# Kernel optimization log

Hardware: AMD Instinct MI355X
Metric: run time of the kernel (lower is better)

The kernel has to match this reference:

```python
import jax, jax.numpy as jnp
import numpy as np

H, F, K, R = 8, 64, 10, 256  # num_heads, in_features, num_sines, num_realizations
B, L = 4, 2048


def setup_inputs() -> dict:
    key = jax.random.key(0)
    k1, k2, k3, k4, k5, k6 = jax.random.split(key, 6)
    return {
        "queries": jax.random.normal(k1, (B, L, H, F), dtype=jnp.float32),
        "keys": jax.random.normal(k2, (B, L, H, F), dtype=jnp.float32),
        "z": jax.random.normal(k3, (B, H, F, 2 * K, R), dtype=jnp.float32),
        "freqs": jax.random.normal(k4, (H, F, K), dtype=jnp.float32),
        "offsets": jax.random.normal(k5, (H, F, K), dtype=jnp.float32),
        "gains": jax.random.normal(k6, (H, F, K), dtype=jnp.float32),
    }


def reference(queries, keys, z, freqs, offsets, gains):
    h, f_dim, k_sines = freqs.shape
    length = queries.shape[1]
    r = z.shape[-1]
    # split positional / non-positional features (rest is empty here: key_dim == in_features)
    q_pos, q_rest = queries[..., :f_dim], queries[..., f_dim:]
    k_pos, k_rest = keys[..., :f_dim], keys[..., f_dim:]

    idx = jnp.arange(length, dtype=queries.dtype)  # linspace(0, L-1, L)
    fr = jax.nn.sigmoid(freqs)[:, :, None, :] / 2.0          # [H, F, 1, K]
    base = 2.0 * jnp.pi * fr * idx[None, None, :, None]       # [H, F, L, K]
    ph_q = base + offsets[:, :, None, :]
    ph_k = base
    # stack(cos, sin) on last axis then flatten -> interleaved cos0,sin0,... : [H, F, L, 2K]
    omega_q = jnp.stack([jnp.cos(ph_q), jnp.sin(ph_q)], axis=-1).reshape(h, f_dim, length, 2 * k_sines)
    omega_k = jnp.stack([jnp.cos(ph_k), jnp.sin(ph_k)], axis=-1).reshape(h, f_dim, length, 2 * k_sines)

    g = jnp.tile(jax.nn.softplus(gains), (1, 1, 2))           # [H, F, 2K] (block-repeated, as in torch .repeat)
    zs = z * g[None, :, :, :, None] / np.sqrt(r * f_dim).astype(np.float32)  # [B, H, F, 2K, R]

    # fused double contraction over f (in_features) and s (2K sines); equals
    # (omega @ z) permuted then multiplied by queries and summed over in_features
    qhat = jnp.einsum('hfls,bhfsr,blhf->blhr', omega_q, zs, q_pos)  # [B, L, H, R]
    khat = jnp.einsum('hfls,bhfsr,blhf->blhr', omega_k, zs, k_pos)

    qhat = jnp.concatenate([qhat, q_rest], axis=-1)
    khat = jnp.concatenate([khat, k_rest], axis=-1)
    return qhat, khat
```

## Files before the change

### kernel.cpp

```cpp
#include <hip/hip_runtime.h>
#include <math.h>


#define NH 8
#define NF 64
#define NK 10
#define NR 256
#define NB 4
#define NL 2048
#define KTOT 1280
#define BM 128
#define BK 32
#define NCH (KTOT/BK)
#define NFRAG_B 16
#define WS_NEEDED ((size_t)NB*NH*NCH*NFRAG_B*1024)

typedef __attribute__((ext_vector_type(8))) short short8;
typedef __attribute__((ext_vector_type(4))) float f32x4;
typedef __attribute__((ext_vector_type(4))) unsigned int u32x4;
typedef __attribute__((ext_vector_type(2))) unsigned int u32x2;

static __device__ __forceinline__ unsigned short f2b(float f) {
    unsigned x = __float_as_uint(f);
    return (unsigned short)((x + 0x7FFFu + ((x >> 16) & 1u)) >> 16);
}
static __device__ __forceinline__ unsigned int pk2(float a, float b) {
    return (unsigned int)f2b(a) | ((unsigned int)f2b(b) << 16);
}
static __device__ __forceinline__ unsigned int cvtpk(float lo, float hi) {
    unsigned int r;
    asm("v_cvt_pk_bf16_f32 %0, %1, %2" : "=v"(r) : "v"(lo), "v"(hi));
    return r;
}
static __device__ __forceinline__ void gload_lds16(const void* g, void* l) {
    __builtin_amdgcn_global_load_lds(
        (const __attribute__((address_space(1))) unsigned int*)g,
        (__attribute__((address_space(3))) unsigned int*)l, 16, 0, 0);
}

__global__ __launch_bounds__(256)
void spe_prep(const float* __restrict__ z, const float* __restrict__ gains,
              unsigned char* __restrict__ bpack)
{
    __shared__ float s_g[NF*NK];
    const int ch  = blockIdx.x;
    const int bh  = blockIdx.y;
    const int h   = bh & 7;
    const int tid = threadIdx.x;
    for (int i = tid; i < NF*NK; i += 256)
        s_g[i] = log1pf(expf(gains[h*NF*NK + i])) * 0.0078125f;
    __syncthreads();
    const float* zb = z + (size_t)bh * KTOT * NR;
    unsigned char* dst = bpack + ((size_t)(bh*NCH + ch) * NFRAG_B) * 1024;
    #pragma unroll
    for (int it = 0; it < 4; ++it) {
        const int s  = tid + 256*it;
        const int fi = s >> 6;
        const int l  = s & 63;
        const int r  = fi*16 + (l & 15);
        const int k0 = ch*BK + (l >> 4)*8;
        u32x4 wv;
        #pragma unroll
        for (int jp = 0; jp < 4; ++jp) {
            const int ka = k0 + 2*jp, kb = ka + 1;
            const int fa = (ka*3277) >> 16; int sa = ka - fa*20; if (sa >= NK) sa -= NK;
            const int fb = (kb*3277) >> 16; int sb = kb - fb*20; if (sb >= NK) sb -= NK;
            const float va = zb[(size_t)ka*NR + r] * s_g[fa*NK + sa];
            const float vb = zb[(size_t)kb*NR + r] * s_g[fb*NK + sb];
            wv[jp] = pk2(va, vb);
        }
        *(u32x4*)(dst + (size_t)s*16) = wv;
    }
}

#define OFF_B0  0
#define OFF_B1  16384
#define OFF_A   32768
#define OFF_POS 40960
#define OFF_FR  57344
#define OFF_CO  59904
#define OFF_SO  62464
#define SMEM_SZ 65024

__global__ __launch_bounds__(512, 4)
void spe_main(const float* __restrict__ queries, const float* __restrict__ keys,
              const float* __restrict__ freqs, const float* __restrict__ offsets,
              const unsigned char* __restrict__ bpack, float* __restrict__ out)
{
    __shared__ __attribute__((aligned(16))) unsigned char smem[SMEM_SZ];
    const int tid  = threadIdx.x;
    const int lane = tid & 63;
    const int w    = tid >> 6;
    const int l0   = blockIdx.x * 64;
    const int bh   = blockIdx.y;
    const int b = bh >> 3, h = bh & 7;

    float* ld_fr = (float*)(smem + OFF_FR);
    float* ld_co = (float*)(smem + OFF_CO);
    float* ld_so = (float*)(smem + OFF_SO);
    unsigned short* pos_t = (unsigned short*)(smem + OFF_POS);

    for (int i = tid; i < NF*NK; i += 512) {
        const float fv = freqs[h*NF*NK + i];
        ld_fr[i] = 0.5f / (1.0f + expf(-fv));
        const float xo = __builtin_amdgcn_fractf(offsets[h*NF*NK + i] * 0.15915494309189535f);
        ld_co[i] = __builtin_amdgcn_cosf(xo);
        ld_so[i] = __builtin_amdgcn_sinf(xo);
    }
    {
        const int r  = tid >> 2;
        const int f0 = (tid & 3) * 16;
        const int rl = r & 63;
        const float* src = (r < 64)
            ? queries + ((size_t)((b*NL + l0 + rl)*NH + h))*NF + f0
            : keys    + ((size_t)((b*NL + l0 + rl)*NH + h))*NF + f0;
        unsigned short* pdst = pos_t + ((r >> 6) << 12);
        #pragma unroll
        for (int j = 0; j < 4; ++j) {
            const float4 v = *(const float4*)(src + j*4);
            const int f = f0 + j*4;
            pdst[(f+0)*64 + rl] = f2b(v.x);
            pdst[(f+1)*64 + rl] = f2b(v.y);
            pdst[(f+2)*64 + rl] = f2b(v.z);
            pdst[(f+3)*64 + rl] = f2b(v.w);
        }
    }
    __syncthreads();

    const unsigned char* bp = bpack + (size_t)bh * ((size_t)NCH*NFRAG_B*1024);
    const int fi0 = w*2;
    gload_lds16(bp + (size_t)fi0*1024 + lane*16,       smem + OFF_B0 + (fi0  <<10));
    gload_lds16(bp + (size_t)(fi0+1)*1024 + lane*16,   smem + OFF_B0 + ((fi0+1)<<10));

    const int wm = w >> 2, wn = w & 3;
    f32x4 acc[4][4];
    #pragma unroll
    for (int mi = 0; mi < 4; ++mi)
        #pragma unroll
        for (int ni = 0; ni < 4; ++ni)
            acc[mi][ni] = (f32x4){0.f, 0.f, 0.f, 0.f};

    const int rq   = tid & 63;
    const int oct  = (tid >> 6) & 3;
    const int half = tid >> 8;
    const float lf = (float)(l0 + rq);
    const unsigned short* posq = pos_t;
    const unsigned short* posk = pos_t + 4096;
    const int a_log_q = ((rq >> 4) << 10) + ((oct*16 + (rq & 15)) << 4) + (half << 3);
    const int aw_q = a_log_q ^ (((rq >> 4) & 3) << 5);
    const int aw_k = (a_log_q + 4096) ^ (((rq >> 4) & 3) << 5);

    auto synthA = [&](int t, u32x2& q01, u32x2& k01) {
        #pragma unroll
        for (int p = 0; p < 2; ++p) {
            const int kk   = t*BK + oct*8 + (half*2 + p)*2;
            const int f    = (kk*3277) >> 16;
            const int srem = kk - f*20;
            const int kidx = f*NK + (srem >> 1);
            const float x  = __builtin_amdgcn_fractf(ld_fr[kidx] * lf);
            const float ck = __builtin_amdgcn_cosf(x);
            const float sk = __builtin_amdgcn_sinf(x);
            const float co = ld_co[kidx], so = ld_so[kidx];
            const float cq = ck*co - sk*so;
            const float sq = sk*co + ck*so;
            const float pq = __uint_as_float(((unsigned)posq[f*64 + rq]) << 16);
            const float pk = __uint_as_float(((unsigned)posk[f*64 + rq]) << 16);
            q01[p] = cvtpk(cq*pq, sq*pq);
            k01[p] = cvtpk(ck*pk, sk*pk);
        }
    };

    u32x2 q01, k01;
    synthA(0, q01, k01);

    for (int t = 0; t < NCH; ++t) {
        unsigned char* Bcur = smem + ((t & 1) ? OFF_B1 : OFF_B0);
        unsigned char* Bnxt = smem + ((t & 1) ? OFF_B0 : OFF_B1);

        asm volatile("s_waitcnt vmcnt(0)" ::: "memory");
        __builtin_amdgcn_sched_barrier(0);
        __builtin_amdgcn_s_barrier();

        if (t + 1 < NCH) {
            gload_lds16(bp + (size_t)((t+1)*NFRAG_B + fi0)*1024 + lane*16,
                        Bnxt + (fi0<<10));
            gload_lds16(bp + (size_t)((t+1)*NFRAG_B + fi0+1)*1024 + lane*16,
                        Bnxt + ((fi0+1)<<10));
        }

        *(u32x2*)(smem + OFF_A + aw_q) = q01;
        *(u32x2*)(smem + OFF_A + aw_k) = k01;
        asm volatile("s_waitcnt lgkmcnt(0)" ::: "memory");
        __builtin_amdgcn_sched_barrier(0);
        __builtin_amdgcn_s_barrier();

        short8 bf[4];
        #pragma unroll
        for (int ni = 0; ni < 4; ++ni)
            bf[ni] = *(const short8*)(Bcur + ((wn*4 + ni) << 10) + (lane << 4));

        if (t + 1 < NCH) synthA(t + 1, q01, k01);

        #pragma unroll
        for (int mi = 0; mi < 4; ++mi) {
            const int g    = wm*4 + mi;
            const int aoff = (g << 10) + (lane << 4);
            const short8 af = *(const short8*)(smem + OFF_A + (aoff ^ ((g & 3) << 5)));
            #pragma unroll
            for (int ni = 0; ni < 4; ++ni)
                acc[mi][ni] = __builtin_amdgcn_mfma_f32_16x16x32_bf16(af, bf[ni], acc[mi][ni], 0, 0, 0);
        }
    }

    const size_t qk_off = (size_t)wm * ((size_t)NB*NL*NH*NR);
    const int row_l = (lane >> 4) * 4;
    const int col_r = lane & 15;
    #pragma unroll
    for (int mi = 0; mi < 4; ++mi) {
        const int lg = l0 + mi*16 + row_l;
        #pragma unroll
        for (int ni = 0; ni < 4; ++ni) {
            const int rg = wn*64 + ni*16 + col_r;
            const f32x4 v = acc[mi][ni];
            #pragma unroll
            for (int q = 0; q < 4; ++q)
                out[qk_off + ((size_t)((b*NL + lg + q)*NH + h))*NR + rg] = v[q];
        }
    }
}

#define FOFF_B   0
#define FOFF_A   32768
#define FOFF_POS 49152
#define FOFF_FR  65536
#define FOFF_OFS 68096
#define FOFF_GS  70656
#define FSMEM_SZ 73216

__global__ __launch_bounds__(512, 4)
void spe_mfma_fb(const float* __restrict__ queries, const float* __restrict__ keys,
                 const float* __restrict__ z, const float* __restrict__ freqs,
                 const float* __restrict__ offsets, const float* __restrict__ gains,
                 float* __restrict__ out)
{
    __shared__ __attribute__((aligned(16))) unsigned char smem[FSMEM_SZ];
    const int tid = threadIdx.x, lane = tid & 63;
    const int l0 = blockIdx.x * BM, bh = blockIdx.y;
    const int b = bh >> 3, h = bh & 7, isK = blockIdx.z;
    float* ld_fr = (float*)(smem + FOFF_FR);
    float* ld_of = (float*)(smem + FOFF_OFS);
    float* ld_gs = (float*)(smem + FOFF_GS);
    unsigned short* pos_t = (unsigned short*)(smem + FOFF_POS);
    for (int i = tid; i < NF*NK; i += 512) {
        const float fv = freqs[h*NF*NK + i];
        ld_fr[i] = 0.5f / (1.0f + expf(-fv));
        ld_of[i] = isK ? 0.0f : offsets[h*NF*NK + i] * 0.15915494309189535f;
        ld_gs[i] = log1pf(expf(gains[h*NF*NK + i])) * 0.0078125f;
    }
    {
        const float* pos = isK ? keys : queries;
        #pragma unroll
        for (int i = 0; i < 4; ++i) {
            const int lrow = (tid >> 4) + 32*i;
            const int f0 = (tid & 15) * 4;
            const float4 v = *(const float4*)(pos + ((size_t)((b*NL + l0 + lrow)*NH + h))*NF + f0);
            pos_t[(f0+0)*BM + lrow] = f2b(v.x); pos_t[(f0+1)*BM + lrow] = f2b(v.y);
            pos_t[(f0+2)*BM + lrow] = f2b(v.z); pos_t[(f0+3)*BM + lrow] = f2b(v.w);
        }
    }
    __syncthreads();
    const int w = tid >> 6, wm = w >> 2, wn = w & 3;
    f32x4 acc[4][4];
    #pragma unroll
    for (int mi = 0; mi < 4; ++mi)
        #pragma unroll
        for (int ni = 0; ni < 4; ++ni) acc[mi][ni] = (f32x4){0.f,0.f,0.f,0.f};
    const float* zbh = z + (size_t)(b*NH + h) * ((size_t)KTOT*NR);
    for (int ch = 0; ch < KTOT/64; ++ch) {
        const int fs0 = ch * 64;
        #pragma unroll
        for (int i = 0; i < 4; ++i) {
            const int tau = tid + 512*i, r = tau & 255, krun = tau >> 8;
            const float* zp = zbh + (size_t)(fs0 + krun*8)*NR + r;
            u32x4 wv2;
            #pragma unroll
            for (int jp = 0; jp < 4; ++jp) {
                const int fs = fs0 + krun*8 + 2*jp;
                const int f = (fs*3277) >> 16; const int rem = fs - f*20;
                const int km = (rem >= NK) ? rem - NK : rem;
                const int kn = ((rem+1) >= NK && (rem+1) < 2*NK) ? rem+1-NK : rem+1;
                const float sc0 = ld_gs[f*NK + km], sc1 = ld_gs[f*NK + (kn < NK ? kn : kn-NK)];
                wv2[jp] = pk2(zp[(2*jp)*NR]*sc0, zp[(2*jp+1)*NR]*sc1);
            }
            *(u32x4*)(smem + FOFF_B + ((((krun>>2)*16) + (r>>4)) << 10)
                                    + ((((krun&3)*16) + (r&15)) << 4)) = wv2;
        }
        #pragma unroll
        for (int i = 0; i < 2; ++i) {
            const int tau = tid + 512*i, m = tau & 127, krun = tau >> 7;
            const float lff = (float)(l0 + m);
            u32x4 wv2;
            #pragma unroll
            for (int jp = 0; jp < 4; ++jp) {
                const int fs = fs0 + krun*8 + 2*jp;
                const int f = (fs*3277) >> 16; const int rem = fs - f*20;
                const int kidx = f*NK + (rem >> 1);
                const float x = __builtin_amdgcn_fractf(ld_of[kidx] + ld_fr[kidx]*lff);
                const float c = __builtin_amdgcn_cosf(x), sn = __builtin_amdgcn_sinf(x);
                const float p = __uint_as_float(((unsigned)pos_t[f*BM + m]) << 16);
                wv2[jp] = pk2(c*p, sn*p);
            }
            *(u32x4*)(smem + FOFF_A + ((((krun>>2)*8) + (m>>4)) << 10)
                                    + ((((krun&3)*16) + (m&15)) << 4)) = wv2;
        }
        __syncthreads();
        #pragma unroll
        for (int ks = 0; ks < 2; ++ks) {
            short8 bf[4];
            #pragma unroll
            for (int ni = 0; ni < 4; ++ni)
                bf[ni] = *(const short8*)(smem + FOFF_B + ((ks*16 + wn*4 + ni) << 10) + (lane << 4));
            #pragma unroll
            for (int mi = 0; mi < 4; ++mi) {
                const short8 af = *(const short8*)(smem + FOFF_A + ((ks*8 + wm*4 + mi) << 10) + (lane << 4));
                #pragma unroll
                for (int ni = 0; ni < 4; ++ni)
                    acc[mi][ni] = __builtin_amdgcn_mfma_f32_16x16x32_bf16(af, bf[ni], acc[mi][ni], 0, 0, 0);
            }
        }
        __syncthreads();
    }
    const size_t qk_off = (size_t)isK * ((size_t)NB*NL*NH*NR);
    const int row_l = (lane >> 4) * 4, col_r = lane & 15;
    #pragma unroll
    for (int mi = 0; mi < 4; ++mi) {
        const int lg = l0 + wm*64 + mi*16 + row_l;
        #pragma unroll
        for (int ni = 0; ni < 4; ++ni) {
            const int rg = wn*64 + ni*16 + col_r;
            const f32x4 v = acc[mi][ni];
            #pragma unroll
            for (int q = 0; q < 4; ++q)
                out[qk_off + ((size_t)((b*NL + lg + q)*NH + h))*NR + rg] = v[q];
        }
    }
}

extern "C" void kernel_launch(void* const* d_in, const int* in_sizes, int n_in,
                              void* d_out, int out_size, void* d_ws, size_t ws_size,
                              hipStream_t stream) {
    const float* queries = (const float*)d_in[0];
    const float* keys    = (const float*)d_in[1];
    const float* z       = (const float*)d_in[2];
    const float* freqs   = (const float*)d_in[3];
    const float* offsets = (const float*)d_in[4];
    const float* gains   = (const float*)d_in[5];
    float* out = (float*)d_out;

    if (ws_size >= WS_NEEDED) {
        unsigned char* bpack = (unsigned char*)d_ws;
        spe_prep<<<dim3(NCH, NB*NH), 256, 0, stream>>>(z, gains, bpack);
        spe_main<<<dim3(NL/64, NB*NH), 512, 0, stream>>>(queries, keys, freqs, offsets, bpack, out);
    } else {
        spe_mfma_fb<<<dim3(NL/BM, NB*NH, 2), 512, 0, stream>>>(queries, keys, z, freqs, offsets, gains, out);
    }
}
```

Measured before the change: 126.1 us.

## Triple-buffer B fragments with two-deep prefetch and remap A-synthesis thread layout

New measurement: 127.1 us. No clear change (+0.8%).

```diff
diff --git a/kernel.cpp b/kernel.cpp
--- a/kernel.cpp
+++ b/kernel.cpp
@@ -9,7 +9,6 @@
 #define NB 4
 #define NL 2048
 #define KTOT 1280
-#define BM 128
 #define BK 32
 #define NCH (KTOT/BK)
 #define NFRAG_B 16
@@ -73,14 +72,13 @@
     }
 }
 
-#define OFF_B0  0
-#define OFF_B1  16384
-#define OFF_A   32768
-#define OFF_POS 40960
-#define OFF_FR  57344
-#define OFF_CO  59904
-#define OFF_SO  62464
-#define SMEM_SZ 65024
+#define OFF_B   0
+#define OFF_A   49152
+#define OFF_POS 57344
+#define OFF_FR  73728
+#define OFF_CO  76288
+#define OFF_SO  78848
+#define SMEM_SZ 81408
 
 __global__ __launch_bounds__(512, 4)
 void spe_main(const float* __restrict__ queries, const float* __restrict__ keys,
@@ -129,8 +127,10 @@
 
     const unsigned char* bp = bpack + (size_t)bh * ((size_t)NCH*NFRAG_B*1024);
     const int fi0 = w*2;
-    gload_lds16(bp + (size_t)fi0*1024 + lane*16,       smem + OFF_B0 + (fi0  <<10));
-    gload_lds16(bp + (size_t)(fi0+1)*1024 + lane*16,   smem + OFF_B0 + ((fi0+1)<<10));
+    gload_lds16(bp + (size_t)fi0*1024 + lane*16,                 smem + OFF_B + (fi0  <<10));
+    gload_lds16(bp + (size_t)(fi0+1)*1024 + lane*16,             smem + OFF_B + ((fi0+1)<<10));
+    gload_lds16(bp + (size_t)(NFRAG_B + fi0)*1024 + lane*16,     smem + OFF_B + 16384 + (fi0  <<10));
+    gload_lds16(bp + (size_t)(NFRAG_B + fi0+1)*1024 + lane*16,   smem + OFF_B + 16384 + ((fi0+1)<<10));
 
     const int wm = w >> 2, wn = w & 3;
     f32x4 acc[4][4];
@@ -140,20 +140,19 @@
         for (int ni = 0; ni < 4; ++ni)
             acc[mi][ni] = (f32x4){0.f, 0.f, 0.f, 0.f};
 
-    const int rq   = tid & 63;
-    const int oct  = (tid >> 6) & 3;
-    const int half = tid >> 8;
+    const int rq   = ((w & 1) << 5) | (lane & 31);
+    const int oct  = w >> 1;
+    const int half = lane >> 5;
     const float lf = (float)(l0 + rq);
     const unsigned short* posq = pos_t;
     const unsigned short* posk = pos_t + 4096;
-    const int a_log_q = ((rq >> 4) << 10) + ((oct*16 + (rq & 15)) << 4) + (half << 3);
-    const int aw_q = a_log_q ^ (((rq >> 4) & 3) << 5);
-    const int aw_k = (a_log_q + 4096) ^ (((rq >> 4) & 3) << 5);
+    const int aw_q = OFF_A + ((rq >> 4) << 10) + ((oct*16 + (rq & 15)) << 4) + (half << 3);
+    const int aw_k = aw_q + 4096;
 
     auto synthA = [&](int t, u32x2& q01, u32x2& k01) {
         #pragma unroll
         for (int p = 0; p < 2; ++p) {
-            const int kk   = t*BK + oct*8 + (half*2 + p)*2;
+            const int kk   = t*BK + oct*8 + half*4 + p*2;
             const int f    = (kk*3277) >> 16;
             const int srem = kk - f*20;
             const int kidx = f*NK + (srem >> 1);
@@ -173,43 +172,46 @@
     u32x2 q01, k01;
     synthA(0, q01, k01);
 
+    int bsel  = 0;
+    int bsel2 = 2;
     for (int t = 0; t < NCH; ++t) {
-        unsigned char* Bcur = smem + ((t & 1) ? OFF_B1 : OFF_B0);
-        unsigned char* Bnxt = smem + ((t & 1) ? OFF_B0 : OFF_B1);
-
-        asm volatile("s_waitcnt vmcnt(0)" ::: "memory");
+        if (t < NCH-1) { asm volatile("s_waitcnt vmcnt(2)" ::: "memory"); }
+        else           { asm volatile("s_waitcnt vmcnt(0)" ::: "memory"); }
         __builtin_amdgcn_sched_barrier(0);
         __builtin_amdgcn_s_barrier();
 
-        if (t + 1 < NCH) {
-            gload_lds16(bp + (size_t)((t+1)*NFRAG_B + fi0)*1024 + lane*16,
-                        Bnxt + (fi0<<10));
-            gload_lds16(bp + (size_t)((t+1)*NFRAG_B + fi0+1)*1024 + lane*16,
-                        Bnxt + ((fi0+1)<<10));
-        }
-
-        *(u32x2*)(smem + OFF_A + aw_q) = q01;
-        *(u32x2*)(smem + OFF_A + aw_k) = k01;
+        if (t + 2 < NCH) {
+            unsigned char* Bn = smem + OFF_B + bsel2*16384;
+            gload_lds16(bp + (size_t)((t+2)*NFRAG_B + fi0)*1024 + lane*16,
+                        Bn + (fi0<<10));
+            gload_lds16(bp + (size_t)((t+2)*NFRAG_B + fi0+1)*1024 + lane*16,
+                        Bn + ((fi0+1)<<10));
+        }
+
+        *(u32x2*)(smem + aw_q) = q01;
+        *(u32x2*)(smem + aw_k) = k01;
         asm volatile("s_waitcnt lgkmcnt(0)" ::: "memory");
         __builtin_amdgcn_sched_barrier(0);
         __builtin_amdgcn_s_barrier();
 
+        const unsigned char* Bc = smem + OFF_B + bsel*16384;
         short8 bf[4];
         #pragma unroll
         for (int ni = 0; ni < 4; ++ni)
-            bf[ni] = *(const short8*)(Bcur + ((wn*4 + ni) << 10) + (lane << 4));
+            bf[ni] = *(const short8*)(Bc + ((wn*4 + ni) << 10) + (lane << 4));
 
         if (t + 1 < NCH) synthA(t + 1, q01, k01);
 
         #pragma unroll
         for (int mi = 0; mi < 4; ++mi) {
-            const int g    = wm*4 + mi;
-            const int aoff = (g << 10) + (lane << 4);
-            const short8 af = *(const short8*)(smem + OFF_A + (aoff ^ ((g & 3) << 5)));
+            const short8 af = *(const short8*)(smem + OFF_A + ((wm*4 + mi) << 10) + (lane << 4));
             #pragma unroll
             for (int ni = 0; ni < 4; ++ni)
                 acc[mi][ni] = __builtin_amdgcn_mfma_f32_16x16x32_bf16(af, bf[ni], acc[mi][ni], 0, 0, 0);
         }
+
+        bsel  = (bsel  == 2) ? 0 : bsel  + 1;
+        bsel2 = (bsel2 == 2) ? 0 : bsel2 + 1;
     }
 
     const size_t qk_off = (size_t)wm * ((size_t)NB*NL*NH*NR);
@@ -229,6 +231,7 @@
     }
 }
 
+#define BMF 128
 #define FOFF_B   0
 #define FOFF_A   32768
 #define FOFF_POS 49152
@@ -245,7 +248,7 @@
 {
     __shared__ __attribute__((aligned(16))) unsigned char smem[FSMEM_SZ];
     const int tid = threadIdx.x, lane = tid & 63;
-    const int l0 = blockIdx.x * BM, bh = blockIdx.y;
+    const int l0 = blockIdx.x * BMF, bh = blockIdx.y;
     const int b = bh >> 3, h = bh & 7, isK = blockIdx.z;
     float* ld_fr = (float*)(smem + FOFF_FR);
     float* ld_of = (float*)(smem + FOFF_OFS);
@@ -264,8 +267,8 @@
             const int lrow = (tid >> 4) + 32*i;
             const int f0 = (tid & 15) * 4;
             const float4 v = *(const float4*)(pos + ((size_t)((b*NL + l0 + lrow)*NH + h))*NF + f0);
-            pos_t[(f0+0)*BM + lrow] = f2b(v.x); pos_t[(f0+1)*BM + lrow] = f2b(v.y);
-            pos_t[(f0+2)*BM + lrow] = f2b(v.z); pos_t[(f0+3)*BM + lrow] = f2b(v.w);
+            pos_t[(f0+0)*BMF + lrow] = f2b(v.x); pos_t[(f0+1)*BMF + lrow] = f2b(v.y);
+            pos_t[(f0+2)*BMF + lrow] = f2b(v.z); pos_t[(f0+3)*BMF + lrow] = f2b(v.w);
         }
     }
     __syncthreads();
@@ -307,7 +310,7 @@
                 const int kidx = f*NK + (rem >> 1);
                 const float x = __builtin_amdgcn_fractf(ld_of[kidx] + ld_fr[kidx]*lff);
                 const float c = __builtin_amdgcn_cosf(x), sn = __builtin_amdgcn_sinf(x);
-                const float p = __uint_as_float(((unsigned)pos_t[f*BM + m]) << 16);
+                const float p = __uint_as_float(((unsigned)pos_t[f*BMF + m]) << 16);
                 wv2[jp] = pk2(c*p, sn*p);
             }
             *(u32x4*)(smem + FOFF_A + ((((krun>>2)*8) + (m>>4)) << 10)
@@ -362,6 +365,6 @@
         spe_prep<<<dim3(NCH, NB*NH), 256, 0, stream>>>(z, gains, bpack);
         spe_main<<<dim3(NL/64, NB*NH), 512, 0, stream>>>(queries, keys, freqs, offsets, bpack, out);
     } else {
-        spe_mfma_fb<<<dim3(NL/BM, NB*NH, 2), 512, 0, stream>>>(queries, keys, z, freqs, offsets, gains, out);
-    }
-}
+        spe_mfma_fb<<<dim3(NL/BMF, NB*NH, 2), 512, 0, stream>>>(queries, keys, z, freqs, offsets, gains, out);
+    }
+}
```
